# Performance work log

Hardware: AMD Instinct MI355X
Metric: run time of the kernel (lower is better)

The kernel has to match this reference:

```python
import jax, jax.numpy as jnp
import numpy as np

N = 262144   # cohort size (k_n)
M = 8192     # number of ordinal anchor indices (len(Hj))


def setup_inputs() -> dict:
    key = jax.random.key(0)
    k1, k2, k3, k4, k5 = jax.random.split(key, 5)
    time = jax.random.uniform(k1, (N,), dtype=jnp.float32) * 1000.0
    event = (jax.random.uniform(k2, (N,), dtype=jnp.float32) < 0.3).astype(jnp.float32)
    y_true0 = jnp.stack([time, event], axis=1)          # [N,2] (time, event)
    y_true1 = y_true0                                    # second head labels (unused by loss)
    y_pred0 = jax.random.normal(k3, (N, 1), dtype=jnp.float32) * 0.1  # xbeta head 0
    y_pred1 = jax.random.normal(k4, (N, 1), dtype=jnp.float32) * 0.1  # xbeta head 1
    Hj = jnp.sort(jax.random.randint(k5, (M,), 0, N, dtype=jnp.int32))  # static event indices into sorted order
    log_vars = jnp.zeros((2, 1), dtype=jnp.float32)      # layer weights log_var0, log_var1
    return {"y_true0": y_true0, "y_true1": y_true1, "y_pred0": y_pred0,
            "y_pred1": y_pred1, "Hj": Hj, "log_vars": log_vars}


def reference(y_true0, y_true1, y_pred0, y_pred1, Hj, log_vars):
    n = y_true0.shape[0]
    # top_k with k = n == full descending sort by time
    _, order = jax.lax.top_k(y_true0[:, 0], n)

    # ---- neg_log_pl (Cox negative partial log-likelihood, per-sample vector) ----
    xbeta = y_pred0[order, 0]                 # [N] sorted by descending time
    event = y_true0[order, 1]                 # [N]
    denom = jnp.cumsum(jnp.exp(xbeta))        # risk-set cumulative sum
    lossA = -(event * (xbeta - jnp.log(denom)))  # [N]

    # ---- ordinal_loss0 (pairwise ranking over event indices Hj in sorted order) ----
    # intended math: for each j, for ii >= j: cost += 1 - exp(xbeta[Hj[j]] - xbeta[Hj[ii]])
    xb = y_pred1[order, 0]                    # [N] sorted
    xh = xb[Hj]                               # [M]
    m = Hj.shape[0]
    rec = 1.0 - jnp.exp(xh[:, None] - xh[None, :])   # [M,M] rec[j,ii]
    mask = jnp.triu(jnp.ones((m, m), dtype=bool))    # ii >= j
    cost2 = jnp.sum(jnp.where(mask, rec, 0.0))

    # ---- multi_loss combination with learned log variances ----
    lv0 = log_vars[0, 0]
    lv1 = log_vars[1, 0]
    precision1 = jnp.clip(jnp.exp(-lv1), 0.0, 1.0)
    loss = jnp.sum(lossA + lv0) + (precision1 * cost2 + lv1)
    return loss


if __name__ == "__main__":
    out = reference(**setup_inputs())
    print(out)
```

## Files before the change

kernel.cpp:

```cpp
#include <hip/hip_runtime.h>
#include <math.h>


#define NB (1 << 18)
#define BLK 256
#define M40 ((1ull << 40) - 1)

#define STORE_F32_A(p, v) __hip_atomic_store((p), (v), __ATOMIC_RELAXED, __HIP_MEMORY_SCOPE_AGENT)
#define STORE_U64_A(p, v) __hip_atomic_store((unsigned long long*)(p), (v), __ATOMIC_RELAXED, __HIP_MEMORY_SCOPE_AGENT)
#define LOAD_U64_A(p) __hip_atomic_load((const unsigned long long*)(p), __ATOMIC_RELAXED, __HIP_MEMORY_SCOPE_AGENT)
#define LOAD_F32_A(p) __hip_atomic_load((const float*)(p), __ATOMIC_RELAXED, __HIP_MEMORY_SCOPE_AGENT)
#define FADD_U32_A(p, v) __hip_atomic_fetch_add((p), (v), __ATOMIC_RELAXED, __HIP_MEMORY_SCOPE_AGENT)

__device__ __forceinline__ int lin_bucket(float t) {
  int b = (int)(t * 256.0f);
  if (b < 0) b = 0;
  if (b > NB - 1) b = NB - 1;
  return b;
}

__global__ void __launch_bounds__(BLK, 4)
k_hist(const float2* __restrict__ yt0, const float* __restrict__ yp0,
       const int* __restrict__ Hj, int n, int m, int tot,
       unsigned long long* __restrict__ rec, unsigned* __restrict__ seq,
       unsigned* __restrict__ bitmap) {
  int i = blockIdx.x * BLK + threadIdx.x;
  if (i < n) {
    float2 te = yt0[i];
    float e = expf(yp0[i]);
    int b = lin_bucket(te.x);
    unsigned long long qe = (unsigned long long)(e * 16777216.0f + 0.5f);
    if (qe > (1ull << 32)) qe = (1ull << 32);
    unsigned long long ret = atomicAdd(&rec[b], (1ull << 40) | qe);
    seq[i] = (unsigned)(ret >> 40);
  }
  for (int j = i; j < m; j += tot) {
    int h = Hj[j];
    atomicOr(&bitmap[h >> 5], 1u << (h & 31));
  }
}

__global__ void __launch_bounds__(BLK, 4)
k_scan(const unsigned long long* __restrict__ rec,
       unsigned long long* __restrict__ pub,
       unsigned long long* __restrict__ Epack) {
  __shared__ unsigned su[BLK];
  __shared__ float    sf[BLK];
  const int t = threadIdx.x, g = blockIdx.x;

  unsigned cK[4]; float fK[4];
  unsigned runc = 0u; float runf = 0.f;
  #pragma unroll
  for (int k = 0; k < 4; ++k) {
    int b = NB - 1 - (g * 1024 + t * 4 + k);
    unsigned long long v = rec[b];
    cK[k] = (unsigned)(v >> 40);
    fK[k] = (float)((double)(v & M40) * (1.0 / 16777216.0));
    runc += cK[k]; runf += fK[k];
  }
  su[t] = runc; sf[t] = runf;
  __syncthreads();
  for (int off2 = 1; off2 < BLK; off2 <<= 1) {
    unsigned uc = (t >= off2) ? su[t - off2] : 0u;
    float    uf = (t >= off2) ? sf[t - off2] : 0.f;
    __syncthreads();
    su[t] += uc; sf[t] += uf;
    __syncthreads();
  }
  if (t == BLK - 1)
    STORE_U64_A(&pub[g], (1ull << 63) |
                ((unsigned long long)(su[t] & 0x7FFFFFFFu) << 32) |
                (unsigned long long)__float_as_uint(sf[t]));
  unsigned thrC = (t > 0) ? su[t - 1] : 0u;
  float    thrF = (t > 0) ? sf[t - 1] : 0.f;
  __syncthreads();

  unsigned pc = 0u; float pf = 0.f;
  for (int j = t; j < g; j += BLK) {
    unsigned long long v;
    int guard = 0;
    while (!(((v = LOAD_U64_A(&pub[j])) >> 63) & 1ull)) {
      __builtin_amdgcn_s_sleep(1);
      if (++guard > 5000000) break;
    }
    pc += (unsigned)((v >> 32) & 0x7FFFFFFFu);
    pf += __uint_as_float((unsigned)v);
  }
  su[t] = pc; sf[t] = pf;
  __syncthreads();
  for (int s = BLK / 2; s > 0; s >>= 1) {
    if (t < s) { su[t] += su[t + s]; sf[t] += sf[t + s]; }
    __syncthreads();
  }
  const unsigned baseC = su[0]; const float baseF = sf[0];
  __syncthreads();

  unsigned preC = 0u; float preF = 0.f;
  #pragma unroll
  for (int k = 0; k < 4; ++k) {
    int b = NB - 1 - (g * 1024 + t * 4 + k);
    unsigned sfxC = baseC + thrC + preC;
    float    sfxF = baseF + thrF + preF;
    Epack[b] = ((unsigned long long)__float_as_uint(sfxF) << 32) | sfxC;
    preC += cK[k]; preF += fK[k];
  }
}

__global__ void __launch_bounds__(BLK, 4)
k_scatter(const float2* __restrict__ yt0, const float* __restrict__ yp0, int n,
          const unsigned* __restrict__ seq,
          const unsigned long long* __restrict__ Epack,
          uint2* __restrict__ skey2, unsigned* __restrict__ sidx) {
  int i = blockIdx.x * BLK + threadIdx.x;
  if (i >= n) return;
  float2 te = yt0[i];
  unsigned key = __float_as_uint(te.x);
  unsigned ev = (te.y != 0.f) ? 0x80000000u : 0u;
  int b = lin_bucket(te.x);
  unsigned start = ((const unsigned*)Epack)[2u * (unsigned)b];
  float e = expf(yp0[i]);
  unsigned pos = start + seq[i];
  uint2 v; v.x = key; v.y = __float_as_uint(e);
  skey2[pos] = v;
  sidx[pos] = (unsigned)i | ev;
}

__global__ void __launch_bounds__(BLK, 4)
k_main(const float* __restrict__ yp1, const int* __restrict__ Hj,
       const float* __restrict__ lv, int n, int m,
       const unsigned* __restrict__ bitmap,
       const unsigned long long* __restrict__ Epack,
       const uint2* __restrict__ skey2, const unsigned* __restrict__ sidx,
       float* __restrict__ xh, double* __restrict__ accum,
       unsigned* __restrict__ doneCnt, float* __restrict__ out) {
  __shared__ double sd[BLK];
  __shared__ float  wt[4];
  __shared__ int    lastFlag;
  const int t = threadIdx.x;
  int p = blockIdx.x * BLK + t;
  double contrib = 0.0;
  if (p < n) {
    uint2 kv = skey2[p];
    unsigned key = kv.x;
    float e = __uint_as_float(kv.y);
    unsigned sidv = sidx[p];
    unsigned idx = sidv & 0x7FFFFFFFu;
    bool evb = (sidv >> 31) != 0u;
    int b = lin_bucket(__uint_as_float(key));
    unsigned long long ep = Epack[b];
    unsigned start = (unsigned)ep;
    float cross = __uint_as_float((unsigned)(ep >> 32));
    unsigned end = (b > 0) ? ((const unsigned*)Epack)[2u * (unsigned)(b - 1)]
                           : (unsigned)n;
    if (end > (unsigned)n) end = (unsigned)n;
    if (start > end) start = end;
    float wsum = 0.f;
    unsigned wcnt = 0u;
    if (end - start > 1u) {
      for (unsigned q = start; q < end; ++q) {
        uint2 v = skey2[q];
        if (v.x > key) { wsum += __uint_as_float(v.y); wcnt++; }
        else if (v.x == key && (sidx[q] & 0x7FFFFFFFu) < idx) {
          wsum += __uint_as_float(v.y); wcnt++;
        }
      }
    }
    float denom = cross + wsum + e;
    int rank = (int)(start + wcnt);
    if (evb) contrib = (double)logf(denom / e);
    if ((bitmap[rank >> 5] >> (rank & 31)) & 1u) {
      int lo = 0, hi = m;
      while (lo < hi) { int mid = (lo + hi) >> 1; if (Hj[mid] < rank) lo = mid + 1; else hi = mid; }
      if (lo < m && Hj[lo] == rank) {
        float xb1 = yp1[idx];
        for (int j = lo; j < m && Hj[j] == rank; ++j) STORE_F32_A(&xh[j], xb1);
      }
    }
  }
  sd[t] = contrib;
  __syncthreads();
  for (int s = 128; s > 0; s >>= 1) { if (t < s) sd[t] += sd[t + s]; __syncthreads(); }
  if (t == 0) {
    double old = atomicAdd(accum, sd[0]);
    unsigned long long ob = __double_as_longlong(old);
    asm volatile("" :: "v"(ob));
    unsigned r = FADD_U32_A(doneCnt, 1u);
    lastFlag = (r == gridDim.x - 1u) ? 1 : 0;
  }
  __syncthreads();
  if (lastFlag == 0) return;

  {
    int lane = t & 63;
    int w = t >> 6;
    double acc = 0.0;
    float carry = 0.f;
    int passes = (m + 2047) / 2048;
    for (int pss = passes - 1; pss >= 0; --pss) {
      int base = pss * 2048 + t * 8;
      float x[8], eb[8];
      float c = 0.f;
      #pragma unroll
      for (int k = 0; k < 8; ++k) {
        int j = base + k;
        x[k] = (j < m) ? LOAD_F32_A(&xh[j]) : 0.f;
        eb[k] = (j < m) ? expf(-x[k]) : 0.f;
        c += eb[k];
      }
      float s = c;
      #pragma unroll
      for (int d = 1; d < 64; d <<= 1) {
        float o = __shfl_down(s, d, 64);
        if (lane + d < 64) s += o;
      }
      float wtot = __shfl(s, 0, 64);
      if (lane == 0) wt[w] = wtot;
      __syncthreads();
      float after = 0.f, ptot = 0.f;
      #pragma unroll
      for (int w2 = 0; w2 < 4; ++w2) { ptot += wt[w2]; if (w2 > w) after += wt[w2]; }
      float S = (s - c) + after + carry;
      #pragma unroll
      for (int k = 7; k >= 0; --k) {
        int j = base + k;
        S += eb[k];
        if (j < m) acc += (double)(expf(x[k]) * S);
      }
      __syncthreads();
      carry += ptot;
    }
    sd[t] = acc;
    __syncthreads();
    for (int s2 = 128; s2 > 0; s2 >>= 1) { if (t < s2) sd[t] += sd[t + s2]; __syncthreads(); }
    if (t == 0) {
      double T = (double)m * (double)(m + 1) * 0.5;
      double cost2 = T - sd[0];
      float lv0 = lv[0], lv1 = lv[1];
      float prec1 = fminf(expf(-lv1), 1.0f);
      double av = __longlong_as_double((long long)LOAD_U64_A(accum));
      double loss = av + (double)n * (double)lv0 + (double)prec1 * cost2 + (double)lv1;
      out[0] = (float)loss;
    }
  }
}

extern "C" void kernel_launch(void* const* d_in, const int* in_sizes, int n_in,
                              void* d_out, int out_size, void* d_ws, size_t ws_size,
                              hipStream_t stream) {
  (void)n_in; (void)out_size;
  const float2* yt0 = (const float2*)d_in[0];
  const float*  yp0 = (const float*)d_in[2];
  const float*  yp1 = (const float*)d_in[3];
  const int*    Hj  = (const int*)d_in[4];
  const float*  lv  = (const float*)d_in[5];
  int n = in_sizes[0] / 2;
  int m = in_sizes[4];

  char* ws = (char*)d_ws;
  size_t off = 0;
  auto alloc = [&](size_t bytes) -> void* {
    void* p = ws + off;
    off += (bytes + 255) & ~(size_t)255;
    return p;
  };
  double*   accum   = (double*)alloc(128);
  unsigned* doneCnt = (unsigned*)alloc(128);
  size_t nbm = ((size_t)(n + 31) / 32) * 4;
  unsigned* bitmap  = (unsigned*)alloc(nbm);
  unsigned long long* pub = (unsigned long long*)alloc((NB / 1024) * 8);
  unsigned long long* rec = (unsigned long long*)alloc((size_t)NB * 8);
  size_t zbytes = off;
  unsigned long long* Epack = (unsigned long long*)alloc((size_t)NB * 8);
  unsigned* seq   = (unsigned*)alloc((size_t)n * 4);
  uint2*    skey2 = (uint2*)alloc((size_t)n * 8);
  unsigned* sidx  = (unsigned*)alloc((size_t)n * 4);
  float*    xh    = (float*)alloc((size_t)m * 4);
  if (off > ws_size) return;

  hipMemsetAsync(ws, 0, zbytes, stream);

  int gN = (n + BLK - 1) / BLK;
  int tot = gN * BLK;
  int gS = NB / 1024;
  k_hist<<<dim3(gN), dim3(BLK), 0, stream>>>(yt0, yp0, Hj, n, m, tot,
                                             rec, seq, bitmap);
  k_scan<<<dim3(gS), dim3(BLK), 0, stream>>>(rec, pub, Epack);
  k_scatter<<<dim3(gN), dim3(BLK), 0, stream>>>(yt0, yp0, n, seq, Epack,
                                                skey2, sidx);
  k_main<<<dim3(gN), dim3(BLK), 0, stream>>>(yp1, Hj, lv, n, m,
                                             bitmap, Epack, skey2, sidx,
                                             xh, accum, doneCnt,
                                             (float*)d_out);
}
```

Measured before the change: 125.0 us.

## Fuse histogram, scan and scatter into one persistent kernel with grid barriers

Replaces three separate launches (histogram, bucket scan, scatter) with one cooperative-style kernel of 1024 blocks that uses a two-level software grid barrier between phases. Per-element key, event flag, exp value and sequence number are kept in registers across the barriers, so the seq array is no longer written and re-read and expf is not recomputed. This removes two kernel launch gaps and their global round trips. In exchange it depends on all 1024 blocks being co-resident, which is checked once through an occupancy query, and it adds spin-wait barrier latency.

```diff
diff --git a/kernel.cpp b/kernel.cpp
--- a/kernel.cpp
+++ b/kernel.cpp
@@ -4,10 +4,15 @@
 
 #define NB (1 << 18)
 #define BLK 256
+#define NC1 32
 #define M40 ((1ull << 40) - 1)
-
+#define BAR_FLAG 512
+#define BAR_REL  1024
+
+#define STORE_U32_A(p, v) __hip_atomic_store((p), (v), __ATOMIC_RELAXED, __HIP_MEMORY_SCOPE_AGENT)
 #define STORE_F32_A(p, v) __hip_atomic_store((p), (v), __ATOMIC_RELAXED, __HIP_MEMORY_SCOPE_AGENT)
 #define STORE_U64_A(p, v) __hip_atomic_store((unsigned long long*)(p), (v), __ATOMIC_RELAXED, __HIP_MEMORY_SCOPE_AGENT)
+#define LOAD_U32_A(p) __hip_atomic_load((const unsigned*)(p), __ATOMIC_RELAXED, __HIP_MEMORY_SCOPE_AGENT)
 #define LOAD_U64_A(p) __hip_atomic_load((const unsigned long long*)(p), __ATOMIC_RELAXED, __HIP_MEMORY_SCOPE_AGENT)
 #define LOAD_F32_A(p) __hip_atomic_load((const float*)(p), __ATOMIC_RELAXED, __HIP_MEMORY_SCOPE_AGENT)
 #define FADD_U32_A(p, v) __hip_atomic_fetch_add((p), (v), __ATOMIC_RELAXED, __HIP_MEMORY_SCOPE_AGENT)
@@ -17,6 +22,146 @@
   if (b < 0) b = 0;
   if (b > NB - 1) b = NB - 1;
   return b;
+}
+
+template <int GRID>
+__device__ __forceinline__ void gbar(unsigned* bar, unsigned gv) {
+  __syncthreads();
+  constexpr unsigned BPC = GRID / NC1;
+  const int t = threadIdx.x;
+  const unsigned grp = blockIdx.x & (NC1 - 1);
+  if (blockIdx.x == 0) {
+    if (t == 0) {
+      unsigned a = FADD_U32_A(bar + grp * 16, 1u);
+      if (a == gv * BPC - 1u) STORE_U32_A(bar + BAR_FLAG + grp * 16, gv);
+    }
+    if (t < NC1) {
+      int guard = 0;
+      while (LOAD_U32_A(bar + BAR_FLAG + t * 16) < gv) {
+        __builtin_amdgcn_s_sleep(1);
+        if (++guard > 5000000) break;
+      }
+      STORE_U32_A(bar + BAR_REL + t * 16, gv);
+    }
+    __syncthreads();
+  } else {
+    if (t == 0) {
+      unsigned a = FADD_U32_A(bar + grp * 16, 1u);
+      if (a == gv * BPC - 1u) STORE_U32_A(bar + BAR_FLAG + grp * 16, gv);
+      int guard = 0;
+      while (LOAD_U32_A(bar + BAR_REL + grp * 16) < gv) {
+        __builtin_amdgcn_s_sleep(1);
+        if (++guard > 5000000) break;
+      }
+    }
+    __syncthreads();
+  }
+}
+
+template <int GRID>
+__global__ void __launch_bounds__(BLK, 4)
+k_front(const float2* __restrict__ yt0, const float* __restrict__ yp0,
+        const int* __restrict__ Hj, int n, int m,
+        unsigned* __restrict__ bar,
+        unsigned long long* __restrict__ rec,
+        unsigned long long* __restrict__ pub,
+        unsigned* __restrict__ bitmap,
+        unsigned long long* __restrict__ Epack,
+        uint2* __restrict__ skey2, unsigned* __restrict__ sidx) {
+  __shared__ unsigned su[BLK];
+  __shared__ float    sf[BLK];
+  const int t = threadIdx.x, g = blockIdx.x;
+  const int gtid = g * BLK + t;
+
+  unsigned keyR = 0u, evR = 0u, seqR = 0u; float eR = 0.f;
+  if (gtid < n) {
+    float2 te = yt0[gtid];
+    keyR = __float_as_uint(te.x);
+    evR = (te.y != 0.f) ? 0x80000000u : 0u;
+    eR = expf(yp0[gtid]);
+    int b = lin_bucket(te.x);
+    unsigned long long qe = (unsigned long long)(eR * 16777216.0f + 0.5f);
+    if (qe > (1ull << 32)) qe = (1ull << 32);
+    unsigned long long ret = atomicAdd(&rec[b], (1ull << 40) | qe);
+    seqR = (unsigned)(ret >> 40);
+  }
+  for (int j = gtid; j < m; j += GRID * BLK) {
+    int h = Hj[j];
+    atomicOr(&bitmap[h >> 5], 1u << (h & 31));
+  }
+  gbar<GRID>(bar, 1);
+
+  if (g < NB / 1024) {
+    unsigned cK[4]; float fK[4];
+    unsigned runc = 0u; float runf = 0.f;
+    #pragma unroll
+    for (int k = 0; k < 4; ++k) {
+      int b = NB - 1 - (g * 1024 + t * 4 + k);
+      unsigned long long v = rec[b];
+      cK[k] = (unsigned)(v >> 40);
+      fK[k] = (float)((double)(v & M40) * (1.0 / 16777216.0));
+      runc += cK[k]; runf += fK[k];
+    }
+    su[t] = runc; sf[t] = runf;
+    __syncthreads();
+    for (int off2 = 1; off2 < BLK; off2 <<= 1) {
+      unsigned uc = (t >= off2) ? su[t - off2] : 0u;
+      float    uf = (t >= off2) ? sf[t - off2] : 0.f;
+      __syncthreads();
+      su[t] += uc; sf[t] += uf;
+      __syncthreads();
+    }
+    if (t == BLK - 1)
+      STORE_U64_A(&pub[g], (1ull << 63) |
+                  ((unsigned long long)(su[t] & 0x7FFFFFFFu) << 32) |
+                  (unsigned long long)__float_as_uint(sf[t]));
+    unsigned thrC = (t > 0) ? su[t - 1] : 0u;
+    float    thrF = (t > 0) ? sf[t - 1] : 0.f;
+    __syncthreads();
+
+    unsigned pc = 0u; float pf = 0.f;
+    for (int j = t; j < g; j += BLK) {
+      unsigned long long v;
+      int guard = 0;
+      while (!(((v = LOAD_U64_A(&pub[j])) >> 63) & 1ull)) {
+        __builtin_amdgcn_s_sleep(1);
+        if (++guard > 5000000) break;
+      }
+      pc += (unsigned)((v >> 32) & 0x7FFFFFFFu);
+      pf += __uint_as_float((unsigned)v);
+    }
+    su[t] = pc; sf[t] = pf;
+    __syncthreads();
+    for (int s = BLK / 2; s > 0; s >>= 1) {
+      if (t < s) { su[t] += su[t + s]; sf[t] += sf[t + s]; }
+      __syncthreads();
+    }
+    const unsigned baseC = su[0]; const float baseF = sf[0];
+    __syncthreads();
+
+    unsigned preC = 0u; float preF = 0.f;
+    #pragma unroll
+    for (int k = 0; k < 4; ++k) {
+      int b = NB - 1 - (g * 1024 + t * 4 + k);
+      unsigned sfxC = baseC + thrC + preC;
+      float    sfxF = baseF + thrF + preF;
+      STORE_U64_A(&Epack[b],
+                  ((unsigned long long)__float_as_uint(sfxF) << 32) | sfxC);
+      preC += cK[k]; preF += fK[k];
+    }
+  }
+  gbar<GRID>(bar, 2);
+
+  if (gtid < n) {
+    unsigned b = (unsigned)lin_bucket(__uint_as_float(keyR));
+    unsigned start = ((const unsigned*)Epack)[2u * b];
+    unsigned pos = start + seqR;
+    if (pos < (unsigned)n) {
+      STORE_U64_A(&skey2[pos],
+                  ((unsigned long long)__float_as_uint(eR) << 32) | keyR);
+      STORE_U32_A(&sidx[pos], (unsigned)gtid | evR);
+    }
+  }
 }
 
 __global__ void __launch_bounds__(BLK, 4)
@@ -47,7 +192,6 @@
   __shared__ unsigned su[BLK];
   __shared__ float    sf[BLK];
   const int t = threadIdx.x, g = blockIdx.x;
-
   unsigned cK[4]; float fK[4];
   unsigned runc = 0u; float runf = 0.f;
   #pragma unroll
@@ -74,7 +218,6 @@
   unsigned thrC = (t > 0) ? su[t - 1] : 0u;
   float    thrF = (t > 0) ? sf[t - 1] : 0.f;
   __syncthreads();
-
   unsigned pc = 0u; float pf = 0.f;
   for (int j = t; j < g; j += BLK) {
     unsigned long long v;
@@ -94,7 +237,6 @@
   }
   const unsigned baseC = su[0]; const float baseF = sf[0];
   __syncthreads();
-
   unsigned preC = 0u; float preF = 0.f;
   #pragma unroll
   for (int k = 0; k < 4; ++k) {
@@ -120,9 +262,11 @@
   unsigned start = ((const unsigned*)Epack)[2u * (unsigned)b];
   float e = expf(yp0[i]);
   unsigned pos = start + seq[i];
-  uint2 v; v.x = key; v.y = __float_as_uint(e);
-  skey2[pos] = v;
-  sidx[pos] = (unsigned)i | ev;
+  if (pos < (unsigned)n) {
+    uint2 v; v.x = key; v.y = __float_as_uint(e);
+    skey2[pos] = v;
+    sidx[pos] = (unsigned)i | ev;
+  }
 }
 
 __global__ void __launch_bounds__(BLK, 4)
@@ -265,6 +409,7 @@
   };
   double*   accum   = (double*)alloc(128);
   unsigned* doneCnt = (unsigned*)alloc(128);
+  unsigned* bar     = (unsigned*)alloc(8192);
   size_t nbm = ((size_t)(n + 31) / 32) * 4;
   unsigned* bitmap  = (unsigned*)alloc(nbm);
   unsigned long long* pub = (unsigned long long*)alloc((NB / 1024) * 8);
@@ -282,11 +427,28 @@
   int gN = (n + BLK - 1) / BLK;
   int tot = gN * BLK;
   int gS = NB / 1024;
-  k_hist<<<dim3(gN), dim3(BLK), 0, stream>>>(yt0, yp0, Hj, n, m, tot,
-                                             rec, seq, bitmap);
-  k_scan<<<dim3(gS), dim3(BLK), 0, stream>>>(rec, pub, Epack);
-  k_scatter<<<dim3(gN), dim3(BLK), 0, stream>>>(yt0, yp0, n, seq, Epack,
-                                                skey2, sidx);
+
+  static int fusedOK = 0;
+  if (fusedOK == 0) {
+    int nb = 0;
+    hipError_t e1 = hipOccupancyMaxActiveBlocksPerMultiprocessor(&nb, k_front<1024>, BLK, 0);
+    int dev = 0; hipGetDevice(&dev);
+    hipDeviceProp_t prop;
+    hipError_t e2 = hipGetDeviceProperties(&prop, dev);
+    fusedOK = (e1 == hipSuccess && e2 == hipSuccess &&
+               nb * prop.multiProcessorCount >= 1024) ? 1 : -1;
+  }
+
+  if (gN == 1024 && fusedOK == 1) {
+    k_front<1024><<<dim3(1024), dim3(BLK), 0, stream>>>(
+        yt0, yp0, Hj, n, m, bar, rec, pub, bitmap, Epack, skey2, sidx);
+  } else {
+    k_hist<<<dim3(gN), dim3(BLK), 0, stream>>>(yt0, yp0, Hj, n, m, tot,
+                                               rec, seq, bitmap);
+    k_scan<<<dim3(gS), dim3(BLK), 0, stream>>>(rec, pub, Epack);
+    k_scatter<<<dim3(gN), dim3(BLK), 0, stream>>>(yt0, yp0, n, seq, Epack,
+                                                  skey2, sidx);
+  }
   k_main<<<dim3(gN), dim3(BLK), 0, stream>>>(yp1, Hj, lv, n, m,
                                              bitmap, Epack, skey2, sidx,
                                              xh, accum, doneCnt,
```

Result: slower. 128.2 us (+2.5%).
